# Kernel optimization log

Hardware: AMD Instinct MI355X
Metric: run time of the kernel (lower is better)

Reference implementation:

```python
import jax, jax.numpy as jnp
import numpy as np

B = 16
CLS_OUT = 80
SCORE_THR = 0.05
IOU_THR = 0.65
MAX_NUM = 100
# FPN levels for a 1280x1280 input: (H, W, stride)
LEVELS = [(160, 160, 8), (80, 80, 16), (40, 40, 32)]
N = sum(h * w for h, w, _ in LEVELS)  # 33600


def make_priors():
    # mmdet MlvlPointGenerator(with_stride=True, offset=0): [x*stride, y*stride, stride, stride]
    ps = []
    for h, w, s in LEVELS:
        ys, xs = np.meshgrid(np.arange(h, dtype=np.float32), np.arange(w, dtype=np.float32), indexing='ij')
        st = np.full((h, w), float(s), dtype=np.float32)
        ps.append(np.stack([xs * s, ys * s, st, st], -1).reshape(-1, 4))
    return jnp.asarray(np.concatenate(ps, 0))


def setup_inputs() -> dict:
    key = jax.random.key(0)
    k1, k2, k3 = jax.random.split(key, 3)
    return {
        'cls_scores': jax.random.normal(k1, (B, N, CLS_OUT), dtype=jnp.float32),
        'bbox_preds': jax.random.normal(k2, (B, N, 4), dtype=jnp.float32),
        'objectness': jax.random.normal(k3, (B, N), dtype=jnp.float32),
        'priors': make_priors(),  # [N, 4]
    }


def _bbox_decode(priors, bbox_preds):
    # xy = pred_xy * stride + center;  wh = exp(pred_wh) * stride
    xys = bbox_preds[..., :2] * priors[:, 2:] + priors[:, :2]
    whs = jnp.exp(bbox_preds[..., 2:]) * priors[:, 2:]
    tl = xys - whs * 0.5
    br = xys + whs * 0.5
    return jnp.concatenate([tl, br], axis=-1)  # [B, N, 4] as (x1, y1, x2, y2)


def _iou_matrix(b1, b2):
    # b1: [M,4], b2: [M,4] -> [M,M], matching torch_cal_bbox_ious (no +1 offsets, eps=1e-8)
    x1 = jnp.maximum(b1[:, None, 0], b2[None, :, 0])
    y1 = jnp.maximum(b1[:, None, 1], b2[None, :, 1])
    x2 = jnp.minimum(b1[:, None, 2], b2[None, :, 2])
    y2 = jnp.minimum(b1[:, None, 3], b2[None, :, 3])
    inter = jnp.clip(x2 - x1, 0.0) * jnp.clip(y2 - y1, 0.0)
    a1 = (b1[:, 2] - b1[:, 0]) * (b1[:, 3] - b1[:, 1])
    a2 = (b2[:, 2] - b2[:, 0]) * (b2[:, 3] - b2[:, 1])
    union = a1[:, None] + a2[None, :] - inter
    return inter / (union + 1e-8)


def _nms_single(boxes, scores, labels, valid):
    # Take top MAX_NUM by score (invalid -> -inf), then class-aware greedy suppression.
    masked = jnp.where(valid, scores, -jnp.inf)
    order = jnp.argsort(-masked)[:MAX_NUM]
    b = boxes[order]          # [M,4]
    s = scores[order]         # [M]
    l = labels[order]         # [M]
    v = valid[order]          # [M]
    iou = _iou_matrix(b, b)
    same = l[:, None] == l[None, :]
    idx = jnp.arange(MAX_NUM)

    def body(i, keep):
        sup = keep[i] & same[i] & (iou[i] >= IOU_THR) & (idx > i)
        return keep & ~sup

    keep = jax.lax.fori_loop(0, MAX_NUM, body, v)
    dets = jnp.where(keep[:, None], jnp.concatenate([b, s[:, None]], -1), 0.0)  # [M,5]
    labs = jnp.where(keep, l, -1)
    return dets, labs, keep


def reference(cls_scores, bbox_preds, objectness, priors):
    cls = jax.nn.sigmoid(cls_scores)                  # [B,N,C]
    obj = jax.nn.sigmoid(objectness)                  # [B,N]
    bboxes = _bbox_decode(priors, bbox_preds)         # [B,N,4]
    max_scores = jnp.max(cls, axis=-1)                # [B,N]
    labels = jnp.argmax(cls, axis=-1).astype(jnp.int32)
    scores = max_scores * obj
    valid = scores >= SCORE_THR
    dets, labs, keep = jax.vmap(_nms_single)(bboxes, scores, labels, valid)
    out = jnp.concatenate([dets, labs[..., None].astype(jnp.float32)], -1)  # [B,MAX_NUM,6]
    return out, keep
```

## Files before the change

kernel.cpp:

```cpp
#include <hip/hip_runtime.h>
#include <cstddef>
#include <cstdint>

#define BB 16
#define NN 33600
#define CC 80
#define MAXN 100
#define NBINS 4096
#define MAXC 1024
#define SCORE_THR_F 0.05f
#define IOU_THR_F 0.65f

#define NCHUNK 525
#define K1_CPB 4
#define K1_GX ((NCHUNK + K1_CPB - 1) / K1_CPB)
#define K2T 512

__global__ __launch_bounds__(256) void k1_score(const float* __restrict__ cls,
                                                const float* __restrict__ obj,
                                                float* __restrict__ masked) {
  const int b = blockIdx.y;
  const int q = threadIdx.x & 3;
  const int r = threadIdx.x >> 2;
  const int c_end = min(blockIdx.x * K1_CPB + K1_CPB, NCHUNK);
  for (int c = blockIdx.x * K1_CPB; c < c_end; c++) {
    const int n = c * 64 + r;
    const float4* row = (const float4*)(cls + ((size_t)b * NN + n) * CC);
    float m = -INFINITY;
#pragma unroll
    for (int j = 0; j < 5; j++) {
      float4 v = row[q + 4 * j];
      m = fmaxf(m, fmaxf(fmaxf(v.x, v.y), fmaxf(v.z, v.w)));
    }
#pragma unroll
    for (int d = 1; d < 4; d <<= 1) m = fmaxf(m, __shfl_xor(m, d, 4));
    if (q == 0) {
      float o = obj[(size_t)b * NN + n];
      float s = (1.0f / (1.0f + expf(-m))) * (1.0f / (1.0f + expf(-o)));
      masked[(size_t)b * NN + n] = (s >= SCORE_THR_F) ? s : -INFINITY;
    }
  }
}

__device__ __forceinline__ int score_bin(float s) {
  return min(NBINS - 1, (int)(s * (float)NBINS));
}

__global__ __launch_bounds__(K2T) void k2_all(const float* __restrict__ cls,
                                              const float* __restrict__ bbox,
                                              const float* __restrict__ priors,
                                              const float* __restrict__ masked,
                                              float* __restrict__ out) {
  const int b = blockIdx.x;
  const int tid = threadIdx.x;

  __shared__ int hist[NBINS];
  __shared__ int sfx[K2T];
  __shared__ int s_t, s_cnt;
  __shared__ float cs[MAXC];
  __shared__ int ci[MAXC];
  __shared__ int sel[MAXN];
  __shared__ float sb[MAXN][4];
  __shared__ float ssc[MAXN];
  __shared__ int slab[MAXN];
  __shared__ unsigned int sup[MAXN][4];
  __shared__ unsigned int keepw[4];

  const float4* msc4 = (const float4*)(masked + (size_t)b * NN);

  for (int i = tid; i < NBINS; i += K2T) hist[i] = 0;
  if (tid == 0) { s_t = 0; s_cnt = 0; }
  __syncthreads();

  for (int i = tid; i < NN / 4; i += K2T) {
    float4 v = msc4[i];
    if (v.x >= SCORE_THR_F) atomicAdd(&hist[score_bin(v.x)], 1);
    if (v.y >= SCORE_THR_F) atomicAdd(&hist[score_bin(v.y)], 1);
    if (v.z >= SCORE_THR_F) atomicAdd(&hist[score_bin(v.z)], 1);
    if (v.w >= SCORE_THR_F) atomicAdd(&hist[score_bin(v.w)], 1);
  }
  __syncthreads();

  int sum = 0;
#pragma unroll
  for (int j = 0; j < NBINS / K2T; j++) sum += hist[tid * (NBINS / K2T) + j];
  sfx[tid] = sum;
  __syncthreads();
  for (int off = 1; off < K2T; off <<= 1) {
    int v = sfx[tid];
    int add = (tid + off < K2T) ? sfx[tid + off] : 0;
    __syncthreads();
    sfx[tid] = v + add;
    __syncthreads();
  }
  {
    int Sc = sfx[tid];
    int Sn = (tid < K2T - 1) ? sfx[tid + 1] : 0;
    if (Sc >= MAXN && Sn < MAXN) {
      int running = Sn;
      const int lo = tid * (NBINS / K2T);
      for (int bin = lo + (NBINS / K2T) - 1; bin >= lo; bin--) {
        running += hist[bin];
        if (running >= MAXN) { s_t = bin; break; }
      }
    }
  }
  __syncthreads();
  const int t = s_t;

  for (int i = tid; i < NN / 4; i += K2T) {
    float4 v = msc4[i];
    int base = i * 4;
    if (v.x >= SCORE_THR_F && score_bin(v.x) >= t) {
      int p = atomicAdd(&s_cnt, 1); if (p < MAXC) { cs[p] = v.x; ci[p] = base; }
    }
    if (v.y >= SCORE_THR_F && score_bin(v.y) >= t) {
      int p = atomicAdd(&s_cnt, 1); if (p < MAXC) { cs[p] = v.y; ci[p] = base + 1; }
    }
    if (v.z >= SCORE_THR_F && score_bin(v.z) >= t) {
      int p = atomicAdd(&s_cnt, 1); if (p < MAXC) { cs[p] = v.z; ci[p] = base + 2; }
    }
    if (v.w >= SCORE_THR_F && score_bin(v.w) >= t) {
      int p = atomicAdd(&s_cnt, 1); if (p < MAXC) { cs[p] = v.w; ci[p] = base + 3; }
    }
  }
  __syncthreads();
  const int C = min(s_cnt, MAXC);

  for (int k = tid; k < MAXN; k += K2T) sel[k] = -1;
  __syncthreads();

  for (int i = tid; i < C; i += K2T) {
    float si = cs[i]; int ii = ci[i];
    int r = 0;
    for (int j = 0; j < C; j++) {
      float sj = cs[j]; int ij = ci[j];
      r += (sj > si) || (sj == si && ij < ii);
    }
    if (r < MAXN) { sel[r] = ii; ssc[r] = si; }
  }
  __syncthreads();

  if (tid < MAXN) {
    int idx = sel[tid];
    if (idx >= 0) {
      float4 p = ((const float4*)priors)[idx];
      float4 d = ((const float4*)bbox)[(size_t)b * NN + idx];
      float cx = d.x * p.z + p.x;
      float cy = d.y * p.w + p.y;
      float hw = expf(d.z) * p.z * 0.5f;
      float hh = expf(d.w) * p.w * 0.5f;
      sb[tid][0] = cx - hw; sb[tid][1] = cy - hh;
      sb[tid][2] = cx + hw; sb[tid][3] = cy + hh;
      const float4* crow = (const float4*)(cls + ((size_t)b * NN + idx) * CC);
      float m = -INFINITY; int lab = 0;
#pragma unroll 4
      for (int j = 0; j < CC / 4; j++) {
        float4 v = crow[j];
        int c0 = 4 * j;
        if (v.x > m) { m = v.x; lab = c0; }
        if (v.y > m) { m = v.y; lab = c0 + 1; }
        if (v.z > m) { m = v.z; lab = c0 + 2; }
        if (v.w > m) { m = v.w; lab = c0 + 3; }
      }
      slab[tid] = lab;
    } else {
      sb[tid][0] = 0.f; sb[tid][1] = 0.f; sb[tid][2] = 0.f; sb[tid][3] = 0.f;
      ssc[tid] = 0.f; slab[tid] = -1;
    }
  }
  for (int i = tid; i < MAXN * 4; i += K2T) ((unsigned int*)sup)[i] = 0;
  __syncthreads();

  for (int p = tid; p < MAXN * MAXN; p += K2T) {
    int i = p / MAXN, j = p % MAXN;
    if (j > i && sel[i] >= 0 && sel[j] >= 0 && slab[i] == slab[j]) {
      float xx1 = fmaxf(sb[i][0], sb[j][0]);
      float yy1 = fmaxf(sb[i][1], sb[j][1]);
      float xx2 = fminf(sb[i][2], sb[j][2]);
      float yy2 = fminf(sb[i][3], sb[j][3]);
      float inter = fmaxf(xx2 - xx1, 0.f) * fmaxf(yy2 - yy1, 0.f);
      float ai = (sb[i][2] - sb[i][0]) * (sb[i][3] - sb[i][1]);
      float aj = (sb[j][2] - sb[j][0]) * (sb[j][3] - sb[j][1]);
      float iou = inter / (ai + aj - inter + 1e-8f);
      if (iou >= IOU_THR_F) atomicOr(&sup[i][j >> 5], 1u << (j & 31));
    }
  }
  __syncthreads();

  if (tid == 0) {
    unsigned int kw0 = 0, kw1 = 0, kw2 = 0, kw3 = 0;
    for (int k = 0; k < MAXN; k++)
      if (sel[k] >= 0) {
        if (k < 32) kw0 |= 1u << k;
        else if (k < 64) kw1 |= 1u << (k - 32);
        else if (k < 96) kw2 |= 1u << (k - 64);
        else kw3 |= 1u << (k - 96);
      }
    for (int i = 0; i < MAXN; i++) {
      unsigned int bit = (i < 32) ? (kw0 >> i) : (i < 64) ? (kw1 >> (i - 32))
                        : (i < 96) ? (kw2 >> (i - 64)) : (kw3 >> (i - 96));
      if (bit & 1u) {
        kw0 &= ~sup[i][0]; kw1 &= ~sup[i][1];
        kw2 &= ~sup[i][2]; kw3 &= ~sup[i][3];
      }
    }
    keepw[0] = kw0; keepw[1] = kw1; keepw[2] = kw2; keepw[3] = kw3;
  }
  __syncthreads();

  if (tid < MAXN) {
    int k = tid;
    bool kp = (keepw[k >> 5] >> (k & 31)) & 1u;
    float* row = out + ((size_t)b * MAXN + k) * 6;
    if (kp) {
      row[0] = sb[k][0]; row[1] = sb[k][1]; row[2] = sb[k][2]; row[3] = sb[k][3];
      row[4] = ssc[k];   row[5] = (float)slab[k];
    } else {
      row[0] = 0.f; row[1] = 0.f; row[2] = 0.f; row[3] = 0.f;
      row[4] = 0.f; row[5] = -1.f;
    }
    out[(size_t)BB * MAXN * 6 + (size_t)b * MAXN + k] = kp ? 1.0f : 0.0f;
  }
}

extern "C" void kernel_launch(void* const* d_in, const int* in_sizes, int n_in,
                              void* d_out, int out_size, void* d_ws, size_t ws_size,
                              hipStream_t stream) {
  const float* cls    = (const float*)d_in[0];
  const float* bbox   = (const float*)d_in[1];
  const float* obj    = (const float*)d_in[2];
  const float* priors = (const float*)d_in[3];
  float* out = (float*)d_out;
  float* masked = (float*)d_ws;

  k1_score<<<dim3(K1_GX, BB), 256, 0, stream>>>(cls, obj, masked);
  k2_all<<<BB, K2T, 0, stream>>>(cls, bbox, priors, masked, out);
}
```

Baseline: 292.2 us.

## Compute argmax labels in score kernel, widen NMS block, use wave-level scans

```diff
diff --git a/kernel.cpp b/kernel.cpp
--- a/kernel.cpp
+++ b/kernel.cpp
@@ -14,30 +14,45 @@
 #define NCHUNK 525
 #define K1_CPB 4
 #define K1_GX ((NCHUNK + K1_CPB - 1) / K1_CPB)
-#define K2T 512
+#define K2T 1024
+#define BPT (NBINS / K2T)
+
+typedef float f4 __attribute__((ext_vector_type(4)));
 
 __global__ __launch_bounds__(256) void k1_score(const float* __restrict__ cls,
                                                 const float* __restrict__ obj,
-                                                float* __restrict__ masked) {
+                                                float* __restrict__ masked,
+                                                unsigned char* __restrict__ labels) {
   const int b = blockIdx.y;
   const int q = threadIdx.x & 3;
   const int r = threadIdx.x >> 2;
   const int c_end = min(blockIdx.x * K1_CPB + K1_CPB, NCHUNK);
   for (int c = blockIdx.x * K1_CPB; c < c_end; c++) {
     const int n = c * 64 + r;
-    const float4* row = (const float4*)(cls + ((size_t)b * NN + n) * CC);
+    const f4* row = (const f4*)(cls + ((size_t)b * NN + n) * CC);
     float m = -INFINITY;
+    int lab = 0;
 #pragma unroll
     for (int j = 0; j < 5; j++) {
-      float4 v = row[q + 4 * j];
-      m = fmaxf(m, fmaxf(fmaxf(v.x, v.y), fmaxf(v.z, v.w)));
-    }
-#pragma unroll
-    for (int d = 1; d < 4; d <<= 1) m = fmaxf(m, __shfl_xor(m, d, 4));
+      f4 v = __builtin_nontemporal_load(row + q + 4 * j);
+      const int c0 = (q + 4 * j) * 4;
+      if (v.x > m) { m = v.x; lab = c0; }
+      if (v.y > m) { m = v.y; lab = c0 + 1; }
+      if (v.z > m) { m = v.z; lab = c0 + 2; }
+      if (v.w > m) { m = v.w; lab = c0 + 3; }
+    }
+#pragma unroll
+    for (int d = 1; d < 4; d <<= 1) {
+      float m2 = __shfl_xor(m, d, 4);
+      int l2 = __shfl_xor(lab, d, 4);
+      if (m2 > m || (m2 == m && l2 < lab)) { m = m2; lab = l2; }
+    }
     if (q == 0) {
-      float o = obj[(size_t)b * NN + n];
+      const size_t bn = (size_t)b * NN + n;
+      float o = obj[bn];
       float s = (1.0f / (1.0f + expf(-m))) * (1.0f / (1.0f + expf(-o)));
-      masked[(size_t)b * NN + n] = (s >= SCORE_THR_F) ? s : -INFINITY;
+      masked[bn] = (s >= SCORE_THR_F) ? s : -INFINITY;
+      labels[bn] = (unsigned char)lab;
     }
   }
 }
@@ -46,16 +61,18 @@
   return min(NBINS - 1, (int)(s * (float)NBINS));
 }
 
-__global__ __launch_bounds__(K2T) void k2_all(const float* __restrict__ cls,
-                                              const float* __restrict__ bbox,
+__global__ __launch_bounds__(K2T) void k2_all(const float* __restrict__ bbox,
                                               const float* __restrict__ priors,
                                               const float* __restrict__ masked,
+                                              const unsigned char* __restrict__ labels,
                                               float* __restrict__ out) {
   const int b = blockIdx.x;
   const int tid = threadIdx.x;
+  const int lane = tid & 63;
+  const int wv = tid >> 6;
 
   __shared__ int hist[NBINS];
-  __shared__ int sfx[K2T];
+  __shared__ int wtot[K2T / 64];
   __shared__ int s_t, s_cnt;
   __shared__ float cs[MAXC];
   __shared__ int ci[MAXC];
@@ -64,16 +81,18 @@
   __shared__ float ssc[MAXN];
   __shared__ int slab[MAXN];
   __shared__ unsigned int sup[MAXN][4];
-  __shared__ unsigned int keepw[4];
-
-  const float4* msc4 = (const float4*)(masked + (size_t)b * NN);
+  __shared__ unsigned long long keep_lo, keep_hi;
+
+  const f4* msc4 = (const f4*)(masked + (size_t)b * NN);
 
   for (int i = tid; i < NBINS; i += K2T) hist[i] = 0;
+  for (int i = tid; i < MAXN * 4; i += K2T) ((unsigned int*)sup)[i] = 0;
+  if (tid < MAXN) sel[tid] = -1;
   if (tid == 0) { s_t = 0; s_cnt = 0; }
   __syncthreads();
 
   for (int i = tid; i < NN / 4; i += K2T) {
-    float4 v = msc4[i];
+    f4 v = msc4[i];
     if (v.x >= SCORE_THR_F) atomicAdd(&hist[score_bin(v.x)], 1);
     if (v.y >= SCORE_THR_F) atomicAdd(&hist[score_bin(v.y)], 1);
     if (v.z >= SCORE_THR_F) atomicAdd(&hist[score_bin(v.z)], 1);
@@ -81,35 +100,33 @@
   }
   __syncthreads();
 
-  int sum = 0;
-#pragma unroll
-  for (int j = 0; j < NBINS / K2T; j++) sum += hist[tid * (NBINS / K2T) + j];
-  sfx[tid] = sum;
-  __syncthreads();
-  for (int off = 1; off < K2T; off <<= 1) {
-    int v = sfx[tid];
-    int add = (tid + off < K2T) ? sfx[tid + off] : 0;
-    __syncthreads();
-    sfx[tid] = v + add;
-    __syncthreads();
-  }
-  {
-    int Sc = sfx[tid];
-    int Sn = (tid < K2T - 1) ? sfx[tid + 1] : 0;
-    if (Sc >= MAXN && Sn < MAXN) {
-      int running = Sn;
-      const int lo = tid * (NBINS / K2T);
-      for (int bin = lo + (NBINS / K2T) - 1; bin >= lo; bin--) {
-        running += hist[bin];
-        if (running >= MAXN) { s_t = bin; break; }
-      }
+  int gsum = 0;
+#pragma unroll
+  for (int j = 0; j < BPT; j++) gsum += hist[tid * BPT + j];
+  int sfx = gsum;
+#pragma unroll
+  for (int off = 1; off < 64; off <<= 1) {
+    int t2 = __shfl_down(sfx, off);
+    if (lane + off < 64) sfx += t2;
+  }
+  if (lane == 0) wtot[wv] = sfx;
+  __syncthreads();
+  int offw = 0;
+#pragma unroll
+  for (int w = 0; w < K2T / 64; w++) offw += (w > wv) ? wtot[w] : 0;
+  const int S = sfx + offw;
+  if (S >= MAXN && S - gsum < MAXN) {
+    int running = S - gsum;
+    for (int bin = tid * BPT + BPT - 1; bin >= tid * BPT; bin--) {
+      running += hist[bin];
+      if (running >= MAXN) { s_t = bin; break; }
     }
   }
   __syncthreads();
   const int t = s_t;
 
   for (int i = tid; i < NN / 4; i += K2T) {
-    float4 v = msc4[i];
+    f4 v = msc4[i];
     int base = i * 4;
     if (v.x >= SCORE_THR_F && score_bin(v.x) >= t) {
       int p = atomicAdd(&s_cnt, 1); if (p < MAXC) { cs[p] = v.x; ci[p] = base; }
@@ -126,9 +143,6 @@
   }
   __syncthreads();
   const int C = min(s_cnt, MAXC);
-
-  for (int k = tid; k < MAXN; k += K2T) sel[k] = -1;
-  __syncthreads();
 
   for (int i = tid; i < C; i += K2T) {
     float si = cs[i]; int ii = ci[i];
@@ -144,32 +158,20 @@
   if (tid < MAXN) {
     int idx = sel[tid];
     if (idx >= 0) {
-      float4 p = ((const float4*)priors)[idx];
-      float4 d = ((const float4*)bbox)[(size_t)b * NN + idx];
+      f4 p = ((const f4*)priors)[idx];
+      f4 d = ((const f4*)bbox)[(size_t)b * NN + idx];
       float cx = d.x * p.z + p.x;
       float cy = d.y * p.w + p.y;
       float hw = expf(d.z) * p.z * 0.5f;
       float hh = expf(d.w) * p.w * 0.5f;
       sb[tid][0] = cx - hw; sb[tid][1] = cy - hh;
       sb[tid][2] = cx + hw; sb[tid][3] = cy + hh;
-      const float4* crow = (const float4*)(cls + ((size_t)b * NN + idx) * CC);
-      float m = -INFINITY; int lab = 0;
-#pragma unroll 4
-      for (int j = 0; j < CC / 4; j++) {
-        float4 v = crow[j];
-        int c0 = 4 * j;
-        if (v.x > m) { m = v.x; lab = c0; }
-        if (v.y > m) { m = v.y; lab = c0 + 1; }
-        if (v.z > m) { m = v.z; lab = c0 + 2; }
-        if (v.w > m) { m = v.w; lab = c0 + 3; }
-      }
-      slab[tid] = lab;
+      slab[tid] = labels[(size_t)b * NN + idx];
     } else {
       sb[tid][0] = 0.f; sb[tid][1] = 0.f; sb[tid][2] = 0.f; sb[tid][3] = 0.f;
       ssc[tid] = 0.f; slab[tid] = -1;
     }
   }
-  for (int i = tid; i < MAXN * 4; i += K2T) ((unsigned int*)sup)[i] = 0;
   __syncthreads();
 
   for (int p = tid; p < MAXN * MAXN; p += K2T) {
@@ -188,30 +190,39 @@
   }
   __syncthreads();
 
-  if (tid == 0) {
-    unsigned int kw0 = 0, kw1 = 0, kw2 = 0, kw3 = 0;
-    for (int k = 0; k < MAXN; k++)
-      if (sel[k] >= 0) {
-        if (k < 32) kw0 |= 1u << k;
-        else if (k < 64) kw1 |= 1u << (k - 32);
-        else if (k < 96) kw2 |= 1u << (k - 64);
-        else kw3 |= 1u << (k - 96);
+  if (tid < 64) {
+    unsigned a0 = sup[lane][0], a1 = sup[lane][1], a2 = sup[lane][2], a3 = sup[lane][3];
+    unsigned b0 = 0, b1 = 0, b2 = 0, b3 = 0;
+    if (lane + 64 < MAXN) {
+      b0 = sup[lane + 64][0]; b1 = sup[lane + 64][1];
+      b2 = sup[lane + 64][2]; b3 = sup[lane + 64][3];
+    }
+    unsigned long long lo = __ballot(sel[lane] >= 0);
+    unsigned long long hi = __ballot(lane + 64 < MAXN && sel[lane + 64] >= 0);
+    for (int i = 0; i < MAXN; i++) {
+      bool kb = (i < 64) ? ((lo >> i) & 1ull) : ((hi >> (i - 64)) & 1ull);
+      if (kb) {
+        unsigned s0, s1, s2, s3;
+        if (i < 64) {
+          s0 = (unsigned)__shfl((int)a0, i); s1 = (unsigned)__shfl((int)a1, i);
+          s2 = (unsigned)__shfl((int)a2, i); s3 = (unsigned)__shfl((int)a3, i);
+        } else {
+          s0 = (unsigned)__shfl((int)b0, i - 64); s1 = (unsigned)__shfl((int)b1, i - 64);
+          s2 = (unsigned)__shfl((int)b2, i - 64); s3 = (unsigned)__shfl((int)b3, i - 64);
+        }
+        lo &= ~(((unsigned long long)s1 << 32) | s0);
+        hi &= ~(((unsigned long long)s3 << 32) | s2);
       }
-    for (int i = 0; i < MAXN; i++) {
-      unsigned int bit = (i < 32) ? (kw0 >> i) : (i < 64) ? (kw1 >> (i - 32))
-                        : (i < 96) ? (kw2 >> (i - 64)) : (kw3 >> (i - 96));
-      if (bit & 1u) {
-        kw0 &= ~sup[i][0]; kw1 &= ~sup[i][1];
-        kw2 &= ~sup[i][2]; kw3 &= ~sup[i][3];
-      }
-    }
-    keepw[0] = kw0; keepw[1] = kw1; keepw[2] = kw2; keepw[3] = kw3;
+    }
+    if (lane == 0) { keep_lo = lo; keep_hi = hi; }
   }
   __syncthreads();
 
   if (tid < MAXN) {
     int k = tid;
-    bool kp = (keepw[k >> 5] >> (k & 31)) & 1u;
+    unsigned long long kw = (k < 64) ? keep_lo : keep_hi;
+    int kbit = (k < 64) ? k : k - 64;
+    bool kp = (kw >> kbit) & 1ull;
     float* row = out + ((size_t)b * MAXN + k) * 6;
     if (kp) {
       row[0] = sb[k][0]; row[1] = sb[k][1]; row[2] = sb[k][2]; row[3] = sb[k][3];
@@ -233,7 +244,8 @@
   const float* priors = (const float*)d_in[3];
   float* out = (float*)d_out;
   float* masked = (float*)d_ws;
-
-  k1_score<<<dim3(K1_GX, BB), 256, 0, stream>>>(cls, obj, masked);
-  k2_all<<<BB, K2T, 0, stream>>>(cls, bbox, priors, masked, out);
-}
+  unsigned char* labels = (unsigned char*)(masked + (size_t)BB * NN);
+
+  k1_score<<<dim3(K1_GX, BB), 256, 0, stream>>>(cls, obj, masked, labels);
+  k2_all<<<BB, K2T, 0, stream>>>(bbox, priors, masked, labels, out);
+}
```

Result: faster. 266.7 us (-8.8%).
